# Kernel optimization log

Hardware: AMD Instinct MI355X
Metric: run time of the kernel (lower is better)

Reference implementation:

```python
import jax, jax.numpy as jnp
import numpy as np
from jax import lax


def _lstm_cell(x, h, c, W_ih, W_hh, b_ih, b_hh):
    # torch nn.LSTMCell: gates = x W_ih^T + b_ih + h W_hh^T + b_hh, order i,f,g,o
    gates = x @ W_ih.T + h @ W_hh.T + (b_ih + b_hh)
    i, f, g, o = jnp.split(gates, 4, axis=-1)
    c_new = jax.nn.sigmoid(f) * c + jax.nn.sigmoid(i) * jnp.tanh(g)
    h_new = jax.nn.sigmoid(o) * jnp.tanh(c_new)
    return h_new, c_new


def setup_inputs():
    key = jax.random.key(0)
    ks = jax.random.split(key, 10)
    B, S, E, H, V = 128, 20, 512, 512, 10000
    images = jax.random.normal(ks[0], (B, E), jnp.float32)
    captions = jax.random.randint(ks[1], (B, S), 0, V)
    length = jax.random.randint(ks[2], (B, 1), 2, S + 1)
    length = length.at[0, 0].set(S)  # guarantee max decode length == S-1 (static shape)
    s = 0.05
    emb = jax.random.normal(ks[3], (V, E), jnp.float32) * s
    W_ih = jax.random.normal(ks[4], (4 * H, E), jnp.float32) * s
    W_hh = jax.random.normal(ks[5], (4 * H, H), jnp.float32) * s
    b_ih = jax.random.normal(ks[6], (4 * H,), jnp.float32) * s
    b_hh = jax.random.normal(ks[7], (4 * H,), jnp.float32) * s
    fc_w = jax.random.normal(ks[8], (V, H), jnp.float32) * s
    fc_b = jax.random.normal(ks[9], (V,), jnp.float32) * s
    return dict(images=images, captions=captions, length=length, emb=emb,
                W_ih=W_ih, W_hh=W_hh, b_ih=b_ih, b_hh=b_hh, fc_w=fc_w, fc_b=fc_b)


def reference(images, captions, length, emb, W_ih, W_hh, b_ih, b_hh, fc_w, fc_b):
    B, S = captions.shape
    T = S - 1  # static max(decode_lengths) by construction
    H = W_hh.shape[1]
    lens = length[:, 0]
    sort_ind = jnp.argsort(-lens)  # stable descending sort, like torch .sort(descending=True)
    sorted_lens = lens[sort_ind]
    dec_len = sorted_lens - 1
    features = images[sort_ind]
    captions_s = captions[sort_ind]
    embeddings = emb[captions_s]  # [B, S, E]

    zeros = jnp.zeros((B, H), images.dtype)
    h, c = _lstm_cell(features, zeros, zeros, W_ih, W_hh, b_ih, b_hh)

    xs = (jnp.swapaxes(embeddings[:, :T, :], 0, 1), jnp.arange(T))  # [T,B,E], [T]

    def step(carry, x):
        h, c = carry
        x_t, t = x
        # ragged batch in the original == masking here: rows with dec_len<=t never
        # contribute to any future valid output (lengths sorted descending).
        h, c = _lstm_cell(x_t, h, c, W_ih, W_hh, b_ih, b_hh)
        preds = h @ fc_w.T + fc_b  # dropout is identity in eval mode
        preds = jnp.where((dec_len > t)[:, None], preds, 0.0)
        return (h, c), preds

    (_, _), preds = lax.scan(step, (h, c), xs)
    predictions = jnp.swapaxes(preds, 0, 1)  # [B, T, V]
    return predictions, captions_s, dec_len, sort_ind
```

## Files before the change

### kernel.cpp

```cpp
#include <hip/hip_runtime.h>

typedef float  f32x4 __attribute__((ext_vector_type(4)));
typedef short  s16x8 __attribute__((ext_vector_type(8)));
typedef unsigned short u16x4 __attribute__((ext_vector_type(4)));

#define MFMA16(a,b,c) __builtin_amdgcn_mfma_f32_16x16x32_bf16(a,b,c,0,0,0)

#define PRED_ELEMS 24320000ull

__device__ __forceinline__ unsigned short f2bf(float f){
  unsigned u = __builtin_bit_cast(unsigned, f);
  u += 0x7fffu + ((u >> 16) & 1u);
  return (unsigned short)(u >> 16);
}
__device__ __forceinline__ float sigf(float x){ return 1.0f/(1.0f + __expf(-x)); }
__device__ __forceinline__ float tanh_(float x){
  x = fminf(15.0f, fmaxf(-15.0f, x));
  float e = __expf(2.0f*x);
  return (e - 1.0f) / (e + 1.0f);
}
__device__ __forceinline__ s16x8 ld8(const unsigned short* p){
  return *reinterpret_cast<const s16x8*>(p);
}
__device__ __forceinline__ void gload_lds16(const unsigned short* src, unsigned short* dst){
  __builtin_amdgcn_global_load_lds(
      (const __attribute__((address_space(1))) void*)src,
      (__attribute__((address_space(3))) void*)dst, 16, 0, 0);
}

__global__ void k0_sort(const int* __restrict__ length, const int* __restrict__ captions,
                        float* __restrict__ out, int* __restrict__ sortp,
                        int* __restrict__ nactp, unsigned int* __restrict__ cnt4k)
{
  __shared__ int sl[128], sdl[128], ssi[128];
  int tid = threadIdx.x;
  for (int k = tid; k < 1024; k += 128) cnt4k[k] = 0u;
  if (tid < 128) sl[tid] = length[tid];
  __syncthreads();
  if (tid < 128){
    int l = sl[tid];
    int rank = 0;
    for (int j = 0; j < 128; ++j){
      int lj = sl[j];
      rank += (lj > l) || (lj == l && j < tid);
    }
    sortp[rank] = tid;
    ssi[rank] = tid;   sdl[rank] = l - 1;
  }
  __syncthreads();
  if (tid < 20){
    int c = 0;
    for (int r = 0; r < 128; ++r) c += (sdl[r] >= tid);
    nactp[tid] = c;
  }
  if (tid < 128){
    const size_t P = PRED_ELEMS;
    int si = ssi[tid];
    for (int t = 0; t < 20; ++t) out[P + tid*20 + t] = (float)captions[si*20 + t];
    out[P + 2560 + tid] = (float)sdl[tid];
    out[P + 2688 + tid] = (float)si;
  }
}

__device__ __forceinline__ void cvt4(unsigned short* dst, const float* src, int u){
  f32x4 v = *reinterpret_cast<const f32x4*>(src + (size_t)u*4);
  u16x4 o;
  o[0]=f2bf(v[0]); o[1]=f2bf(v[1]); o[2]=f2bf(v[2]); o[3]=f2bf(v[3]);
  *reinterpret_cast<u16x4*>(dst + (size_t)u*4) = o;
}

__global__ void k1_convert(const float* __restrict__ images, const int* __restrict__ captions,
    const float* __restrict__ emb, const float* __restrict__ wih, const float* __restrict__ whh,
    const float* __restrict__ bih, const float* __restrict__ bhh, const float* __restrict__ fcw,
    const int* __restrict__ sortp,
    unsigned short* __restrict__ wihb, unsigned short* __restrict__ whhb,
    unsigned short* __restrict__ fcwb, float* __restrict__ biasp,
    unsigned short* __restrict__ xseq, unsigned short* __restrict__ hseq,
    unsigned short* __restrict__ hloc)
{
  const int U0 = 262144;
  const int U1 = 262144;
  const int U2 = 1294336;
  const int U3 = 512;
  const int U4 = 327680;
  const int U5 = 16384;
  const int U6 = 16384;
  const int total = U0+U1+U2+U3+U4+U5+U6;
  for (int i = blockIdx.x*blockDim.x + threadIdx.x; i < total; i += gridDim.x*blockDim.x){
    int j = i;
    if (j < U0){ cvt4(wihb, wih, j); continue; }
    j -= U0;
    if (j < U1){ cvt4(whhb, whh, j); continue; }
    j -= U1;
    if (j < U2){
      int row = j >> 7;
      if (row < 10000) cvt4(fcwb, fcw, j);
      else { u16x4 z = {0,0,0,0}; *reinterpret_cast<u16x4*>(fcwb + (size_t)j*4) = z; }
      continue;
    }
    j -= U2;
    if (j < U3){
      int e0 = j*4;
      for (int e = 0; e < 4; ++e) biasp[e0+e] = bih[e0+e] + bhh[e0+e];
      continue;
    }
    j -= U3;
    if (j < U4){
      int elem = j*4;
      int s = elem >> 16;
      int rem = elem & 65535;
      int r = rem >> 9;
      int k = rem & 511;
      const float* src;
      if (s == 0) src = images + (size_t)sortp[r]*512 + k;
      else {
        int cap = captions[sortp[r]*20 + (s-1)];
        src = emb + (size_t)cap*512 + k;
      }
      f32x4 v = *reinterpret_cast<const f32x4*>(src);
      u16x4 o;
      o[0]=f2bf(v[0]); o[1]=f2bf(v[1]); o[2]=f2bf(v[2]); o[3]=f2bf(v[3]);
      *reinterpret_cast<u16x4*>(xseq + (size_t)j*4) = o;
      continue;
    }
    j -= U4;
    if (j < U5){ u16x4 z = {0,0,0,0}; *reinterpret_cast<u16x4*>(hseq + (size_t)j*4) = z; continue; }
    j -= U5;
    {
      int e0 = j*4;
      int x = e0 >> 13;
      int rem = e0 & 8191;
      u16x4 z = {0,0,0,0};
      *reinterpret_cast<u16x4*>(hloc + (size_t)x*172032 + rem) = z;
    }
  }
}

__global__ __launch_bounds__(256) void lstm_chain(
    const unsigned short* __restrict__ xseq, const unsigned short* __restrict__ wih,
    const unsigned short* __restrict__ whh, const float* __restrict__ biasp,
    unsigned short* __restrict__ hseq, unsigned short* __restrict__ hloc,
    const int* __restrict__ nact, unsigned int* __restrict__ claimc,
    unsigned int* __restrict__ flags)
{
  const int tid = threadIdx.x;
  __shared__ int s_xw;
  __shared__ unsigned short WIl[64*524];
  __shared__ unsigned short WHl[64*524];
  __shared__ float pg[4][4][16][17];

  if (tid == 0){
    unsigned xcc;
    asm volatile("s_getreg_b32 %0, hwreg(20, 0, 4)" : "=s"(xcc));
    int x = (int)(xcc & 7u);
    unsigned slot = __hip_atomic_fetch_add(claimc + x*64, 1u,
                      __ATOMIC_RELAXED, __HIP_MEMORY_SCOPE_AGENT);
    s_xw = (x << 8) | (int)(slot & 255u);
  }
  __syncthreads();
  const int x = s_xw >> 8;
  const int w = s_xw & 255;
  if (w >= 32) return;
  const int R0 = x*16;
  const int C0 = w*16;
  unsigned int* myflags = flags + x*64;

  const int lane = tid & 63;
  const int kk   = tid >> 6;
  const int fr   = lane & 15;
  const int fkq  = (lane >> 4) * 8;

  for (int idx = tid; idx < 64*64; idx += 256){
    int lr = idx >> 6, kc = (idx & 63)*8;
    int q = lr >> 4, jj = lr & 15;
    size_t off = (size_t)(q*512 + C0 + jj)*512 + kc;
    *reinterpret_cast<s16x8*>(&WIl[lr*524 + kc]) = ld8(wih + off);
    *reinterpret_cast<s16x8*>(&WHl[lr*524 + kc]) = ld8(whh + off);
  }

  unsigned short* hl = hloc + (size_t)x*172032;
  const int prow = tid >> 4;
  const int pcol = tid & 15;
  const float bz0 = biasp[       C0 + pcol];
  const float bz1 = biasp[ 512 + C0 + pcol];
  const float bz2 = biasp[1024 + C0 + pcol];
  const float bz3 = biasp[1536 + C0 + pcol];
  float creg = 0.f;
  __syncthreads();

  for (int s = 0; s < 20; ++s){
    if (R0 >= nact[s]) break;
    const unsigned short* hp = hl + (size_t)s*8192;
    const unsigned short* xp = xseq + (size_t)s*65536;

    s16x8 ah[4], ax[4];
    #pragma unroll
    for (int i = 0; i < 4; ++i){
      ah[i] = ld8(hp + fr*512 + kk*128 + i*32 + fkq);
      ax[i] = ld8(xp + (R0 + fr)*512 + kk*128 + i*32 + fkq);
    }

    #pragma unroll
    for (int q = 0; q < 4; ++q){
      f32x4 acc = (f32x4){0.f,0.f,0.f,0.f};
      #pragma unroll
      for (int i = 0; i < 4; ++i){
        s16x8 bi = *reinterpret_cast<const s16x8*>(&WIl[(q*16 + fr)*524 + kk*128 + i*32 + fkq]);
        s16x8 bh = *reinterpret_cast<const s16x8*>(&WHl[(q*16 + fr)*524 + kk*128 + i*32 + fkq]);
        acc = MFMA16(ax[i], bi, acc);
        acc = MFMA16(ah[i], bh, acc);
      }
      const int rr = (lane >> 4) * 4;
      #pragma unroll
      for (int p = 0; p < 4; ++p)
        pg[kk][q][rr + p][fr] = acc[p];
    }
    __syncthreads();

    unsigned short hb;
    {
      float iv = pg[0][0][prow][pcol] + pg[1][0][prow][pcol]
               + pg[2][0][prow][pcol] + pg[3][0][prow][pcol] + bz0;
      float fv = pg[0][1][prow][pcol] + pg[1][1][prow][pcol]
               + pg[2][1][prow][pcol] + pg[3][1][prow][pcol] + bz1;
      float gv = pg[0][2][prow][pcol] + pg[1][2][prow][pcol]
               + pg[2][2][prow][pcol] + pg[3][2][prow][pcol] + bz2;
      float ov = pg[0][3][prow][pcol] + pg[1][3][prow][pcol]
               + pg[2][3][prow][pcol] + pg[3][3][prow][pcol] + bz3;
      creg = sigf(fv)*creg + sigf(iv)*tanh_(gv);
      float h = sigf(ov)*tanh_(creg);
      hb = f2bf(h);
      hl[(size_t)(s+1)*8192 + prow*512 + C0 + pcol] = hb;
    }
    __syncthreads();

    hseq[(size_t)(s+1)*65536 + (R0 + prow)*512 + C0 + pcol] = hb;

    if (s < 19 && nact[s+1] > R0){
      const unsigned tgt = (unsigned)(s + 1);
      if (tid == 0)
        __hip_atomic_store(&myflags[w], tgt, __ATOMIC_RELAXED, __HIP_MEMORY_SCOPE_AGENT);
      if (tid < 64){
        long guard = 0;
        for (;;){
          bool ok = true;
          if (tid < 32)
            ok = (__hip_atomic_load(&myflags[tid], __ATOMIC_RELAXED,
                                    __HIP_MEMORY_SCOPE_AGENT) >= tgt);
          if (__all(ok) || ++guard > (1L << 20)) break;
          __builtin_amdgcn_s_sleep(1);
        }
      }
      __syncthreads();
    }
  }
}

__global__ __launch_bounds__(256) void fc_kernel(
    const unsigned short* __restrict__ hseq, const unsigned short* __restrict__ fcwb,
    const float* __restrict__ fcb, const int* __restrict__ nact,
    float* __restrict__ out)
{
  const int b    = blockIdx.x;
  const int x    = b & 7;
  const int slot = b >> 3;
  const int t    = slot % 19;
  const int p    = x + 8*(slot/19);
  if (p >= 79) return;
  const int v0   = p * 128;
  const int tid  = threadIdx.x;

  __shared__ unsigned short Ab[2][128*64];
  __shared__ unsigned short Bb[2][128*64];

  const unsigned short* Ag = hseq + (size_t)(t + 2)*65536;
  const unsigned short* Bg = fcwb + (size_t)v0*512;
  const int n_t = nact[t + 1];

  const int srow = tid >> 3;
  const int sphy = tid & 7;
  const int wuni = (tid >> 6) << 9;

  #define STAGE(gsrc, lbuf, kt)                                              \
    _Pragma("unroll")                                                        \
    for (int call = 0; call < 4; ++call){                                    \
      int row_ = call*32 + srow;                                             \
      gload_lds16(gsrc + (size_t)row_*512 + (kt)*64 + ((sphy ^ (row_ & 7)) << 3), \
                  lbuf + call*2048 + wuni);                                  \
    }

  const int lane = tid & 63;
  const int wv   = tid >> 6;
  const int wr   = wv >> 1, wc = wv & 1;
  const int fr   = lane & 15;
  const int hi   = lane >> 4;

  f32x4 acc[4][4];
  #pragma unroll
  for (int i = 0; i < 4; ++i)
    #pragma unroll
    for (int j = 0; j < 4; ++j)
      acc[i][j] = (f32x4){0.f,0.f,0.f,0.f};

  STAGE(Ag, Ab[0], 0)
  STAGE(Bg, Bb[0], 0)
  asm volatile("s_waitcnt vmcnt(0)" ::: "memory");
  __syncthreads();

  int cur = 0;
  for (int kt = 0; kt < 8; ++kt){
    if (kt < 7){
      STAGE(Ag, Ab[cur^1], kt+1)
      STAGE(Bg, Bb[cur^1], kt+1)
    }
    const unsigned short* As = Ab[cur];
    const unsigned short* Bs = Bb[cur];
    #pragma unroll
    for (int kk = 0; kk < 2; ++kk){
      const int c = kk*4 + hi;
      s16x8 af[4], bf[4];
      #pragma unroll
      for (int i = 0; i < 4; ++i){
        int row = wr*64 + i*16 + fr;
        af[i] = ld8(As + row*64 + ((c ^ (row & 7)) << 3));
      }
      #pragma unroll
      for (int j = 0; j < 4; ++j){
        int col = wc*64 + j*16 + fr;
        bf[j] = ld8(Bs + col*64 + ((c ^ (col & 7)) << 3));
      }
      #pragma unroll
      for (int i = 0; i < 4; ++i)
        #pragma unroll
        for (int j = 0; j < 4; ++j)
          acc[i][j] = MFMA16(af[i], bf[j], acc[i][j]);
    }
    asm volatile("s_waitcnt vmcnt(0)" ::: "memory");
    __syncthreads();
    cur ^= 1;
  }

  const int rr = hi * 4;
  #pragma unroll
  for (int j = 0; j < 4; ++j){
    int v = v0 + wc*64 + j*16 + fr;
    if (v >= 10000) continue;
    float bb = fcb[v];
    #pragma unroll
    for (int i = 0; i < 4; ++i){
      #pragma unroll
      for (int pp = 0; pp < 4; ++pp){
        int r = wr*64 + i*16 + rr + pp;
        out[(size_t)(r*19 + t)*10000 + v] = (r < n_t) ? (acc[i][j][pp] + bb) : 0.0f;
      }
    }
  }
  #undef STAGE
}

extern "C" void kernel_launch(void* const* d_in, const int* in_sizes, int n_in,
                              void* d_out, int out_size, void* d_ws, size_t ws_size,
                              hipStream_t stream) {
  const float* images   = (const float*)d_in[0];
  const int*   captions = (const int*)  d_in[1];
  const int*   length   = (const int*)  d_in[2];
  const float* emb      = (const float*)d_in[3];
  const float* W_ih     = (const float*)d_in[4];
  const float* W_hh     = (const float*)d_in[5];
  const float* b_ih     = (const float*)d_in[6];
  const float* b_hh     = (const float*)d_in[7];
  const float* fc_w     = (const float*)d_in[8];
  const float* fc_b     = (const float*)d_in[9];
  float* out = (float*)d_out;
  char*  ws  = (char*)d_ws;

  int*            sortp  = (int*)           (ws + 0);
  int*            nactp  = (int*)           (ws + 2048);
  float*          biasp  = (float*)         (ws + 4096);
  unsigned int*   cnt4k  = (unsigned int*)  (ws + 12288);
  unsigned int*   claimc = cnt4k;
  unsigned int*   flags  = cnt4k + 512;
  unsigned short* hloc   = (unsigned short*)(ws + 16384);
  unsigned short* hseq   = (unsigned short*)(ws + 2768896);
  unsigned short* xseq   = (unsigned short*)(ws + 5521408);
  unsigned short* wihb   = (unsigned short*)(ws + 8142848);
  unsigned short* whhb   = (unsigned short*)(ws + 10240000);
  unsigned short* fcwb   = (unsigned short*)(ws + 12337152);

  k0_sort<<<1, 128, 0, stream>>>(length, captions, out, sortp, nactp, cnt4k);
  k1_convert<<<4096, 256, 0, stream>>>(images, captions, emb, W_ih, W_hh, b_ih, b_hh,
                                       fc_w, sortp, wihb, whhb, fcwb, biasp, xseq, hseq, hloc);
  lstm_chain<<<256, 256, 0, stream>>>(xseq, wihb, whhb, biasp, hseq, hloc,
                                      nactp, claimc, flags);
  fc_kernel<<<1520, 256, 0, stream>>>(hseq, fcwb, fc_b, nactp, out);
}
```

Measured before the change: 127.9 us.

## Prefetch next-step input before barrier, split MFMA chains, use atomic RMW flag polling

Moves the per-step embedding loads for step s+1 ahead of the inter-block spin wait so their latency overlaps the barrier. The single dependent MFMA accumulator chain is split into separate input and hidden accumulators to shorten the dependency chain. Flag publish and poll switch to inline-asm global atomic swap and atomic add of zero, which go to L2 instead of possibly hitting stale caches. This adds more live registers and relies on hand-written asm with specific cache-coherence bits.

Result: slower. 143.2 us (+12.0%).

```diff
diff --git a/kernel.cpp b/kernel.cpp
--- a/kernel.cpp
+++ b/kernel.cpp
@@ -186,34 +186,40 @@
   const float bz2 = biasp[1024 + C0 + pcol];
   const float bz3 = biasp[1536 + C0 + pcol];
   float creg = 0.f;
+
+  s16x8 ax[4];
+  #pragma unroll
+  for (int i = 0; i < 4; ++i)
+    ax[i] = ld8(xseq + (R0 + fr)*512 + kk*128 + i*32 + fkq);
   __syncthreads();
 
   for (int s = 0; s < 20; ++s){
     if (R0 >= nact[s]) break;
     const unsigned short* hp = hl + (size_t)s*8192;
-    const unsigned short* xp = xseq + (size_t)s*65536;
-
-    s16x8 ah[4], ax[4];
+
+    s16x8 ah[4];
     #pragma unroll
-    for (int i = 0; i < 4; ++i){
+    for (int i = 0; i < 4; ++i)
       ah[i] = ld8(hp + fr*512 + kk*128 + i*32 + fkq);
-      ax[i] = ld8(xp + (R0 + fr)*512 + kk*128 + i*32 + fkq);
-    }
 
     #pragma unroll
     for (int q = 0; q < 4; ++q){
-      f32x4 acc = (f32x4){0.f,0.f,0.f,0.f};
+      f32x4 accx = (f32x4){0.f,0.f,0.f,0.f};
+      f32x4 acch = (f32x4){0.f,0.f,0.f,0.f};
       #pragma unroll
       for (int i = 0; i < 4; ++i){
         s16x8 bi = *reinterpret_cast<const s16x8*>(&WIl[(q*16 + fr)*524 + kk*128 + i*32 + fkq]);
+        accx = MFMA16(ax[i], bi, accx);
+      }
+      #pragma unroll
+      for (int i = 0; i < 4; ++i){
         s16x8 bh = *reinterpret_cast<const s16x8*>(&WHl[(q*16 + fr)*524 + kk*128 + i*32 + fkq]);
-        acc = MFMA16(ax[i], bi, acc);
-        acc = MFMA16(ah[i], bh, acc);
+        acch = MFMA16(ah[i], bh, acch);
       }
       const int rr = (lane >> 4) * 4;
       #pragma unroll
       for (int p = 0; p < 4; ++p)
-        pg[kk][q][rr + p][fr] = acc[p];
+        pg[kk][q][rr + p][fr] = accx[p] + acch[p];
     }
     __syncthreads();
 
@@ -238,15 +244,28 @@
 
     if (s < 19 && nact[s+1] > R0){
       const unsigned tgt = (unsigned)(s + 1);
-      if (tid == 0)
-        __hip_atomic_store(&myflags[w], tgt, __ATOMIC_RELAXED, __HIP_MEMORY_SCOPE_AGENT);
+      const unsigned short* xp = xseq + (size_t)(s+1)*65536;
+      #pragma unroll
+      for (int i = 0; i < 4; ++i)
+        ax[i] = ld8(xp + (R0 + fr)*512 + kk*128 + i*32 + fkq);
+
+      if (tid == 0){
+        unsigned int* fa = myflags + w;
+        asm volatile("global_atomic_swap %0, %1, off"
+                     :: "v"(fa), "v"(tgt) : "memory");
+      }
       if (tid < 64){
+        unsigned int* pa = myflags + (tid & 31);
         long guard = 0;
         for (;;){
           bool ok = true;
-          if (tid < 32)
-            ok = (__hip_atomic_load(&myflags[tid], __ATOMIC_RELAXED,
-                                    __HIP_MEMORY_SCOPE_AGENT) >= tgt);
+          if (tid < 32){
+            unsigned old;
+            asm volatile("global_atomic_add %0, %1, %2, off sc0\n\t"
+                         "s_waitcnt vmcnt(0)"
+                         : "=v"(old) : "v"(pa), "v"(0u) : "memory");
+            ok = (old >= tgt);
+          }
           if (__all(ok) || ++guard > (1L << 20)) break;
           __builtin_amdgcn_s_sleep(1);
         }
```
